# Kernel optimization log

Hardware: AMD Instinct MI355X
Metric: run time of the kernel (lower is better)

## Reference

```python
import jax, jax.numpy as jnp
import numpy as np

TEMPERATURE = 0.5
EPS = 1e-8  # torch cosine_similarity norm clamp


def setup_inputs() -> dict:
    key = jax.random.key(0)
    k1, k2, k3 = jax.random.split(key, 3)
    N, D = 4096, 256
    z_i = jax.random.normal(k1, (N, D), dtype=jnp.float32)
    z_j = jax.random.normal(k2, (N, D), dtype=jnp.float32)
    weights = jax.random.uniform(k3, (N,), dtype=jnp.float32)
    return {"z_i": z_i, "z_j": z_j, "weights": weights}


def reference(z_i, z_j, weights):
    N = z_i.shape[0]
    z = jnp.concatenate([z_i, z_j], axis=0)  # [2N, D]
    # cosine similarity via normalized matmul (same math as broadcasted F.cosine_similarity)
    norm = jnp.maximum(jnp.linalg.norm(z, axis=1, keepdims=True), EPS)
    zn = z / norm
    sim = zn @ zn.T  # [2N, 2N]
    # positives: diagonals at offsets +N and -N
    sim_ij = jnp.diagonal(sim, offset=N)
    sim_ji = jnp.diagonal(sim, offset=-N)
    positives = jnp.concatenate([sim_ij, sim_ji], axis=0)  # [2N]
    mask = 1.0 - jnp.eye(2 * N, dtype=sim.dtype)
    denominator = jnp.sum(mask * jnp.exp(sim / TEMPERATURE), axis=1)  # [2N]
    numerator = jnp.exp(positives / TEMPERATURE)
    all_losses = -jnp.log(numerator / denominator)  # [2N]
    w2 = jnp.tile(weights, 2)  # weights.repeat(2)
    loss = jnp.sum(all_losses * w2) / jnp.sum(w2)
    return loss
```

## Files before the change

kernel.cpp:

```cpp
#include <hip/hip_runtime.h>
#include <hip/hip_bf16.h>
#include <hip/hip_fp8.h>

#define PN   4096
#define PN2  8192
#define PD   256
#define TILE 128
#define BK   128
#define NBLK (PN2 / TILE)
#define NTRI (NBLK * (NBLK + 1) / 2)

typedef __attribute__((ext_vector_type(4))) float f32x4;
typedef const __attribute__((address_space(1))) void* gas_ptr;
typedef __attribute__((address_space(3))) void* las_ptr;

__global__ __launch_bounds__(256) void normalize_kernel(
    const float* __restrict__ zi, const float* __restrict__ zj,
    unsigned char* __restrict__ zn8, float* __restrict__ pos,
    float* __restrict__ wlws, unsigned* __restrict__ ticket) {
  const int wave = threadIdx.x >> 6;
  const int lane = threadIdx.x & 63;
  const int r = blockIdx.x * 4 + wave;
  float4 a = *(const float4*)(zi + (size_t)r * PD + lane * 4);
  float4 b = *(const float4*)(zj + (size_t)r * PD + lane * 4);
  float si = a.x * a.x + a.y * a.y + a.z * a.z + a.w * a.w;
  float sj = b.x * b.x + b.y * b.y + b.z * b.z + b.w * b.w;
  float d  = a.x * b.x + a.y * b.y + a.z * b.z + a.w * b.w;
  #pragma unroll
  for (int off = 32; off >= 1; off >>= 1) {
    si += __shfl_xor(si, off, 64);
    sj += __shfl_xor(sj, off, 64);
    d  += __shfl_xor(d,  off, 64);
  }
  float ni = fmaxf(sqrtf(si), 1e-8f);
  float nj = fmaxf(sqrtf(sj), 1e-8f);
  if (lane == 0) {
    float p = d / (ni * nj);
    pos[r] = p;
    pos[r + PN] = p;
  }
  float ia = 1.0f / ni, ib = 1.0f / nj;
  union { unsigned u; unsigned char c[4]; } pa, pb;
  pa.c[0] = __hip_cvt_float_to_fp8(a.x * ia, __HIP_SATFINITE, __HIP_E4M3);
  pa.c[1] = __hip_cvt_float_to_fp8(a.y * ia, __HIP_SATFINITE, __HIP_E4M3);
  pa.c[2] = __hip_cvt_float_to_fp8(a.z * ia, __HIP_SATFINITE, __HIP_E4M3);
  pa.c[3] = __hip_cvt_float_to_fp8(a.w * ia, __HIP_SATFINITE, __HIP_E4M3);
  pb.c[0] = __hip_cvt_float_to_fp8(b.x * ib, __HIP_SATFINITE, __HIP_E4M3);
  pb.c[1] = __hip_cvt_float_to_fp8(b.y * ib, __HIP_SATFINITE, __HIP_E4M3);
  pb.c[2] = __hip_cvt_float_to_fp8(b.z * ib, __HIP_SATFINITE, __HIP_E4M3);
  pb.c[3] = __hip_cvt_float_to_fp8(b.w * ib, __HIP_SATFINITE, __HIP_E4M3);
  *(unsigned*)(zn8 + (size_t)r * PD + lane * 4) = pa.u;
  *(unsigned*)(zn8 + (size_t)(r + PN) * PD + lane * 4) = pb.u;
  if (blockIdx.x == 0 && threadIdx.x == 0) {
    wlws[0] = 0.0f; wlws[1] = 0.0f; *ticket = 0u;
  }
}

__global__ __launch_bounds__(256) void simsum_kernel(
    const unsigned char* __restrict__ zn8, float* __restrict__ rowpart) {
  __shared__ char lds[2 * TILE * BK];
  __shared__ float rowacc[TILE];
  __shared__ float colacc[TILE];
  char* As = lds;
  char* Bs = lds + TILE * BK;

  const int tid = threadIdx.x;
  if (tid < TILE) { rowacc[tid] = 0.0f; colacc[tid] = 0.0f; }

  const int idx = (int)((blockIdx.x & 7) * (NTRI / 8) + (blockIdx.x >> 3));
  int bj = (int)((sqrtf(8.0f * (float)idx + 1.0f) - 1.0f) * 0.5f);
  while ((bj + 1) * (bj + 2) / 2 <= idx) ++bj;
  while (bj * (bj + 1) / 2 > idx) --bj;
  const int bi = idx - bj * (bj + 1) / 2;
  const bool diagBlk = (bi == bj);

  const int wave = tid >> 6;
  const int lane = tid & 63;
  const int quad = lane >> 4;
  const int c16  = lane & 15;
  const int rowBase = bi * TILE;
  const int colBase = bj * TILE;
  const int waveRow = (wave >> 1) * 64;
  const int waveCol = (wave & 1) * 64;
  const int subrow = lane >> 3;
  const int slot   = lane & 7;

  f32x4 acc[4][4];
  #pragma unroll
  for (int i = 0; i < 4; ++i)
    #pragma unroll
    for (int j = 0; j < 4; ++j)
      acc[i][j] = (f32x4){0.f, 0.f, 0.f, 0.f};

  const char* BsEff = diagBlk ? As : Bs;

  for (int kt = 0; kt < PD / BK; ++kt) {
    if (kt) __syncthreads();
    #pragma unroll
    for (int p = 0; p < 4; ++p) {
      int issue = wave * 4 + p;
      int rr = issue * 8 + subrow;
      int cc = slot ^ (rr & 7);
      const unsigned char* ga = zn8 + (size_t)(rowBase + rr) * PD + kt * BK + cc * 16;
      __builtin_amdgcn_global_load_lds((gas_ptr)ga, (las_ptr)(As + issue * 1024), 16, 0, 0);
      if (!diagBlk) {
        const unsigned char* gb = zn8 + (size_t)(colBase + rr) * PD + kt * BK + cc * 16;
        __builtin_amdgcn_global_load_lds((gas_ptr)gb, (las_ptr)(Bs + issue * 1024), 16, 0, 0);
      }
    }
    __syncthreads();

    #pragma unroll
    for (int ki = 0; ki < 4; ++ki) {
      const int G  = ki * 2 + (quad >> 1);
      const int h8 = (quad & 1) * 8;
      long a[4], b[4];
      #pragma unroll
      for (int mi = 0; mi < 4; ++mi) {
        int r = waveRow + mi * 16 + c16;
        a[mi] = *(const long*)(As + r * 128 + (((G ^ (r & 7)) << 4) + h8));
      }
      #pragma unroll
      for (int ni = 0; ni < 4; ++ni) {
        int r = waveCol + ni * 16 + c16;
        b[ni] = *(const long*)(BsEff + r * 128 + (((G ^ (r & 7)) << 4) + h8));
      }
      #pragma unroll
      for (int mi = 0; mi < 4; ++mi)
        #pragma unroll
        for (int ni = 0; ni < 4; ++ni)
          acc[mi][ni] = __builtin_amdgcn_mfma_f32_16x16x32_fp8_fp8(a[mi], b[ni], acc[mi][ni], 0, 0, 0);
    }
  }

  float colsum[4] = {0.f, 0.f, 0.f, 0.f};
  #pragma unroll
  for (int mi = 0; mi < 4; ++mi) {
    int lrow = waveRow + mi * 16 + quad * 4;
    float rs[4] = {0.f, 0.f, 0.f, 0.f};
    #pragma unroll
    for (int ni = 0; ni < 4; ++ni) {
      int gcol = colBase + waveCol + ni * 16 + c16;
      #pragma unroll
      for (int t = 0; t < 4; ++t) {
        int grow = rowBase + lrow + t;
        float e = __expf(2.0f * acc[mi][ni][t]);
        if (diagBlk && gcol == grow) e = 0.0f;
        rs[t] += e;
        colsum[ni] += e;
      }
    }
    #pragma unroll
    for (int t = 0; t < 4; ++t) {
      #pragma unroll
      for (int off = 1; off <= 8; off <<= 1) rs[t] += __shfl_xor(rs[t], off, 64);
    }
    if (c16 == 0) {
      #pragma unroll
      for (int t = 0; t < 4; ++t) atomicAdd(&rowacc[lrow + t], rs[t]);
    }
  }
  if (!diagBlk) {
    #pragma unroll
    for (int ni = 0; ni < 4; ++ni) {
      float cs = colsum[ni];
      cs += __shfl_xor(cs, 16, 64);
      cs += __shfl_xor(cs, 32, 64);
      if (quad == 0) atomicAdd(&colacc[waveCol + ni * 16 + c16], cs);
    }
  }

  __syncthreads();
  if (tid < TILE) {
    rowpart[(size_t)bj * PN2 + rowBase + tid] = rowacc[tid];
    if (!diagBlk)
      rowpart[(size_t)bi * PN2 + colBase + tid] = colacc[tid];
  }
}

__global__ __launch_bounds__(256) void finalize_kernel(
    const float* __restrict__ rowpart, const float* __restrict__ pos,
    const float* __restrict__ w, float* __restrict__ wlws,
    unsigned* __restrict__ ticket, float* __restrict__ out) {
  const int tid = threadIdx.x;
  const int r = blockIdx.x * 256 + tid;
  float s = 0.0f;
  #pragma unroll
  for (int x = 0; x < NBLK; ++x) s += rowpart[(size_t)x * PN2 + r];
  float li = logf(s) - 2.0f * pos[r];
  float wi = w[r & (PN - 1)];
  float wl = wi * li, ws = wi;
  #pragma unroll
  for (int off = 32; off >= 1; off >>= 1) {
    wl += __shfl_xor(wl, off, 64);
    ws += __shfl_xor(ws, off, 64);
  }
  __shared__ float pl[4], pw[4];
  const int lane = tid & 63, wv = tid >> 6;
  if (lane == 0) { pl[wv] = wl; pw[wv] = ws; }
  __syncthreads();
  if (tid == 0) {
    atomicAdd(&wlws[0], pl[0] + pl[1] + pl[2] + pl[3]);
    atomicAdd(&wlws[1], pw[0] + pw[1] + pw[2] + pw[3]);
    __threadfence();
    if (atomicAdd(ticket, 1u) == 31) {
      float a = atomicAdd(&wlws[0], 0.0f);
      float b = atomicAdd(&wlws[1], 0.0f);
      out[0] = a / b;
    }
  }
}

extern "C" void kernel_launch(void* const* d_in, const int* in_sizes, int n_in,
                              void* d_out, int out_size, void* d_ws, size_t ws_size,
                              hipStream_t stream) {
  const float* zi = (const float*)d_in[0];
  const float* zj = (const float*)d_in[1];
  const float* w  = (const float*)d_in[2];
  float* out = (float*)d_out;

  unsigned char* zn8 = (unsigned char*)d_ws;
  float* rowpart = (float*)((char*)d_ws + (size_t)PN2 * PD);
  float* pos     = rowpart + (size_t)NBLK * PN2;
  float* wlws    = pos + PN2;
  unsigned* ticket = (unsigned*)(wlws + 2);

  normalize_kernel<<<PN / 4, 256, 0, stream>>>(zi, zj, zn8, pos, wlws, ticket);
  simsum_kernel<<<NTRI, 256, 0, stream>>>(zn8, rowpart);
  finalize_kernel<<<32, 256, 0, stream>>>(rowpart, pos, w, wlws, ticket, out);
}
```

Before: 112.5 us.

## Enlarge similarity tiles to 256 and load full K into LDS at once

The triangular similarity kernel moves from 128x128 tiles with two K-steps to 256x256 tiles. It uses 512 threads and stages the whole 256-byte row depth of both operands in LDS with a single load phase and a 16-way XOR swizzle. Each wave now computes a 128x64 sub-tile, and A fragments are loaded per row-block inside the MFMA loop. The goal is more operand reuse per byte loaded, fewer blocks and partial row sums, and fewer barriers. In exchange it needs about 128KB of LDS per block, allowing only one block per CU. It also launches far fewer blocks (528), which risks poor wave quantization, and it no longer overlaps loads with compute.

```diff
diff --git a/kernel.cpp b/kernel.cpp
--- a/kernel.cpp
+++ b/kernel.cpp
@@ -5,14 +5,20 @@
 #define PN   4096
 #define PN2  8192
 #define PD   256
-#define TILE 128
-#define BK   128
+#define TILE 256
 #define NBLK (PN2 / TILE)
 #define NTRI (NBLK * (NBLK + 1) / 2)
 
 typedef __attribute__((ext_vector_type(4))) float f32x4;
 typedef const __attribute__((address_space(1))) void* gas_ptr;
 typedef __attribute__((address_space(3))) void* las_ptr;
+
+__device__ __forceinline__ void tri_decode(int idx, int& bi, int& bj) {
+  bj = (int)((sqrtf(8.0f * (float)idx + 1.0f) - 1.0f) * 0.5f);
+  while ((bj + 1) * (bj + 2) / 2 <= idx) ++bj;
+  while (bj * (bj + 1) / 2 > idx) --bj;
+  bi = idx - bj * (bj + 1) / 2;
+}
 
 __global__ __launch_bounds__(256) void normalize_kernel(
     const float* __restrict__ zi, const float* __restrict__ zj,
@@ -56,22 +62,19 @@
   }
 }
 
-__global__ __launch_bounds__(256) void simsum_kernel(
+__global__ __launch_bounds__(512, 2) void simsum_kernel(
     const unsigned char* __restrict__ zn8, float* __restrict__ rowpart) {
-  __shared__ char lds[2 * TILE * BK];
+  __shared__ char As[TILE * PD];
+  __shared__ char Bs[TILE * PD];
   __shared__ float rowacc[TILE];
   __shared__ float colacc[TILE];
-  char* As = lds;
-  char* Bs = lds + TILE * BK;
 
   const int tid = threadIdx.x;
   if (tid < TILE) { rowacc[tid] = 0.0f; colacc[tid] = 0.0f; }
 
   const int idx = (int)((blockIdx.x & 7) * (NTRI / 8) + (blockIdx.x >> 3));
-  int bj = (int)((sqrtf(8.0f * (float)idx + 1.0f) - 1.0f) * 0.5f);
-  while ((bj + 1) * (bj + 2) / 2 <= idx) ++bj;
-  while (bj * (bj + 1) / 2 > idx) --bj;
-  const int bi = idx - bj * (bj + 1) / 2;
+  int bi, bj;
+  tri_decode(idx, bi, bj);
   const bool diagBlk = (bi == bj);
 
   const int wave = tid >> 6;
@@ -80,62 +83,55 @@
   const int c16  = lane & 15;
   const int rowBase = bi * TILE;
   const int colBase = bj * TILE;
-  const int waveRow = (wave >> 1) * 64;
-  const int waveCol = (wave & 1) * 64;
-  const int subrow = lane >> 3;
-  const int slot   = lane & 7;
-
-  f32x4 acc[4][4];
-  #pragma unroll
-  for (int i = 0; i < 4; ++i)
+  const int waveRow = (wave >> 2) * 128;
+  const int waveCol = (wave & 3) * 64;
+
+  #pragma unroll
+  for (int p = 0; p < 8; ++p) {
+    int issue = wave * 8 + p;
+    int rr = issue * 4 + quad;
+    int gs = c16 ^ (rr & 15);
+    const unsigned char* ga = zn8 + (size_t)(rowBase + rr) * PD + gs * 16;
+    __builtin_amdgcn_global_load_lds((gas_ptr)ga, (las_ptr)(As + issue * 1024), 16, 0, 0);
+    if (!diagBlk) {
+      const unsigned char* gb = zn8 + (size_t)(colBase + rr) * PD + gs * 16;
+      __builtin_amdgcn_global_load_lds((gas_ptr)gb, (las_ptr)(Bs + issue * 1024), 16, 0, 0);
+    }
+  }
+  __syncthreads();
+
+  const char* BsEff = diagBlk ? As : Bs;
+
+  f32x4 acc[8][4];
+  #pragma unroll
+  for (int i = 0; i < 8; ++i)
     #pragma unroll
     for (int j = 0; j < 4; ++j)
       acc[i][j] = (f32x4){0.f, 0.f, 0.f, 0.f};
 
-  const char* BsEff = diagBlk ? As : Bs;
-
-  for (int kt = 0; kt < PD / BK; ++kt) {
-    if (kt) __syncthreads();
-    #pragma unroll
-    for (int p = 0; p < 4; ++p) {
-      int issue = wave * 4 + p;
-      int rr = issue * 8 + subrow;
-      int cc = slot ^ (rr & 7);
-      const unsigned char* ga = zn8 + (size_t)(rowBase + rr) * PD + kt * BK + cc * 16;
-      __builtin_amdgcn_global_load_lds((gas_ptr)ga, (las_ptr)(As + issue * 1024), 16, 0, 0);
-      if (!diagBlk) {
-        const unsigned char* gb = zn8 + (size_t)(colBase + rr) * PD + kt * BK + cc * 16;
-        __builtin_amdgcn_global_load_lds((gas_ptr)gb, (las_ptr)(Bs + issue * 1024), 16, 0, 0);
-      }
-    }
-    __syncthreads();
-
-    #pragma unroll
-    for (int ki = 0; ki < 4; ++ki) {
-      const int G  = ki * 2 + (quad >> 1);
-      const int h8 = (quad & 1) * 8;
-      long a[4], b[4];
-      #pragma unroll
-      for (int mi = 0; mi < 4; ++mi) {
-        int r = waveRow + mi * 16 + c16;
-        a[mi] = *(const long*)(As + r * 128 + (((G ^ (r & 7)) << 4) + h8));
-      }
-      #pragma unroll
-      for (int ni = 0; ni < 4; ++ni) {
-        int r = waveCol + ni * 16 + c16;
-        b[ni] = *(const long*)(BsEff + r * 128 + (((G ^ (r & 7)) << 4) + h8));
-      }
-      #pragma unroll
-      for (int mi = 0; mi < 4; ++mi)
-        #pragma unroll
-        for (int ni = 0; ni < 4; ++ni)
-          acc[mi][ni] = __builtin_amdgcn_mfma_f32_16x16x32_fp8_fp8(a[mi], b[ni], acc[mi][ni], 0, 0, 0);
+  #pragma unroll
+  for (int ki = 0; ki < 8; ++ki) {
+    const int G  = ki * 2 + (quad >> 1);
+    const int h8 = (quad & 1) * 8;
+    long b[4];
+    #pragma unroll
+    for (int ni = 0; ni < 4; ++ni) {
+      int r = waveCol + ni * 16 + c16;
+      b[ni] = *(const long*)(BsEff + r * 256 + (((G ^ (r & 15)) << 4) + h8));
+    }
+    #pragma unroll
+    for (int mi = 0; mi < 8; ++mi) {
+      int r = waveRow + mi * 16 + c16;
+      long a = *(const long*)(As + r * 256 + (((G ^ (r & 15)) << 4) + h8));
+      #pragma unroll
+      for (int ni = 0; ni < 4; ++ni)
+        acc[mi][ni] = __builtin_amdgcn_mfma_f32_16x16x32_fp8_fp8(a, b[ni], acc[mi][ni], 0, 0, 0);
     }
   }
 
   float colsum[4] = {0.f, 0.f, 0.f, 0.f};
   #pragma unroll
-  for (int mi = 0; mi < 4; ++mi) {
+  for (int mi = 0; mi < 8; ++mi) {
     int lrow = waveRow + mi * 16 + quad * 4;
     float rs[4] = {0.f, 0.f, 0.f, 0.f};
     #pragma unroll
@@ -226,6 +222,6 @@
   unsigned* ticket = (unsigned*)(wlws + 2);
 
   normalize_kernel<<<PN / 4, 256, 0, stream>>>(zi, zj, zn8, pos, wlws, ticket);
-  simsum_kernel<<<NTRI, 256, 0, stream>>>(zn8, rowpart);
+  simsum_kernel<<<NTRI, 512, 0, stream>>>(zn8, rowpart);
   finalize_kernel<<<32, 256, 0, stream>>>(rowpart, pos, w, wlws, ticket, out);
 }
```

Result: faster. 103.1 us (-8.3%).
